# Optimization experiments

Hardware: AMD Instinct MI355X
Metric: run time of the kernel (lower is better)

Reference implementation:

```python
import jax, jax.numpy as jnp
import numpy as np

B, SQ, SE, D, H, DFF = 16, 512, 512, 512, 8, 2048
DH = D // H
EPS = 1e-6


def _ln(x, g, b):
    mu = jnp.mean(x, axis=-1, keepdims=True)
    var = jnp.mean((x - mu) ** 2, axis=-1, keepdims=True)
    return (x - mu) * jax.lax.rsqrt(var + EPS) * g + b


def _mha(v, k, q, mask, wq_w, wq_b, wk_w, wk_b, wv_w, wv_b, do_w, do_b):
    b = q.shape[0]
    def split(t):  # [b, s, D] -> [b, H, s, DH]
        return t.reshape(b, -1, H, DH).transpose(0, 2, 1, 3)
    qh = split(q @ wq_w + wq_b)
    kh = split(k @ wk_w + wk_b)
    vh = split(v @ wv_w + wv_b)
    logits = jnp.einsum('bhqd,bhkd->bhqk', qh, kh) / jnp.sqrt(jnp.float32(DH))
    logits = logits + mask * (-1e9)
    attn = jax.nn.softmax(logits, axis=-1)
    out = jnp.einsum('bhqk,bhkd->bhqd', attn, vh)
    out = out.transpose(0, 2, 1, 3).reshape(b, -1, D)
    # output projection has GELU activation (exact erf, keras default)
    out = jax.nn.gelu(out @ do_w + do_b, approximate=False)
    return out, attn


def setup_inputs() -> dict:
    key = jax.random.key(0)
    ks = jax.random.split(key, 32)
    s = 0.02  # weight scale
    inp = {
        'x': jax.random.normal(ks[0], (B, SQ, D), dtype=jnp.float32),
        'enc_fc': jax.random.normal(ks[1], (B, SE, D), dtype=jnp.float32),
        'enc_ff': jax.random.normal(ks[2], (B, SE, D), dtype=jnp.float32),
        # causal look-ahead mask: 1 where attention is disallowed
        'look_ahead_mask': jnp.triu(jnp.ones((SQ, SQ), jnp.float32), k=1)[None, None],
        # random padding mask over encoder positions (1 = masked)
        'padding_mask': (jax.random.uniform(ks[3], (B, 1, 1, SE)) < 0.1).astype(jnp.float32),
    }
    i = 4
    for p in ('m1', 'm2'):
        for w in ('wq', 'wk', 'wv', 'do'):
            inp[f'{p}_{w}_w'] = jax.random.normal(ks[i], (D, D), dtype=jnp.float32) * s; i += 1
            inp[f'{p}_{w}_b'] = jnp.zeros((D,), jnp.float32)
    inp['ffn_w1'] = jax.random.normal(ks[i], (D, DFF), dtype=jnp.float32) * s; i += 1
    inp['ffn_b1'] = jnp.zeros((DFF,), jnp.float32)
    inp['ffn_w2'] = jax.random.normal(ks[i], (DFF, D), dtype=jnp.float32) * s; i += 1
    inp['ffn_b2'] = jnp.zeros((D,), jnp.float32)
    for ln in ('ln1', 'ln2', 'ln3'):
        inp[f'{ln}_g'] = jnp.ones((D,), jnp.float32)
        inp[f'{ln}_b'] = jnp.zeros((D,), jnp.float32)
    return inp


def reference(x, enc_fc, enc_ff, look_ahead_mask, padding_mask,
              m1_wq_w, m1_wq_b, m1_wk_w, m1_wk_b, m1_wv_w, m1_wv_b, m1_do_w, m1_do_b,
              m2_wq_w, m2_wq_b, m2_wk_w, m2_wk_b, m2_wv_w, m2_wv_b, m2_do_w, m2_do_b,
              ffn_w1, ffn_b1, ffn_w2, ffn_b2,
              ln1_g, ln1_b, ln2_g, ln2_b, ln3_g, ln3_b):
    # self-attention (v=k=q=x), causal mask
    attn1, aw1 = _mha(x, x, x, look_ahead_mask,
                      m1_wq_w, m1_wq_b, m1_wk_w, m1_wk_b, m1_wv_w, m1_wv_b, m1_do_w, m1_do_b)
    out1 = _ln(attn1 + x, ln1_g, ln1_b)  # dropout identity in eval
    # cross-attention: v=enc_ff, k=enc_fc, q=out1, padding mask
    attn2, aw2 = _mha(enc_ff, enc_fc, out1, padding_mask,
                      m2_wq_w, m2_wq_b, m2_wk_w, m2_wk_b, m2_wv_w, m2_wv_b, m2_do_w, m2_do_b)
    out2 = _ln(attn2 + out1, ln2_g, ln2_b)
    # FFN: relu dense -> (dropout identity) -> dense
    ff = jax.nn.relu(out2 @ ffn_w1 + ffn_b1) @ ffn_w2 + ffn_b2
    out3 = _ln(ff + out2, ln3_g, ln3_b)
    return out3, aw1, aw2
```

## Files before the change

### kernel.cpp

```cpp
#include <hip/hip_runtime.h>
#include <stdint.h>
#include <math.h>

typedef unsigned short u16;
typedef __attribute__((ext_vector_type(8))) __bf16 bf16x8;
typedef __attribute__((ext_vector_type(4))) float f32x4;

#define NB 16
#define NSQ 512
#define NSE 512
#define ND 512
#define NH 8
#define NDH 64
#define NDFF 2048

__device__ __forceinline__ u16 f2b(float f) {
  uint32_t u = __float_as_uint(f);
  u = (u + 0x7FFFu + ((u >> 16) & 1u)) >> 16;
  return (u16)u;
}
__device__ __forceinline__ float b2f(uint32_t h) {
  return __uint_as_float(h << 16);
}

__device__ __forceinline__ void gl_lds16(const u16* g, u16* l) {
  __builtin_amdgcn_global_load_lds(
      (const __attribute__((address_space(1))) void*)g,
      (__attribute__((address_space(3))) void*)l, 16, 0, 0);
}

struct Prep {
  const float *x, *fc, *ff;
  u16 *xb, *fcb, *ffb;
  const float* w8[8];
  u16* o8[8];
  const float *w1, *w2;
  u16 *w1t, *w2t;
};

__device__ __forceinline__ void tr32(const float* __restrict__ W,
                                     u16* __restrict__ Wt, int K, int N, int bx,
                                     int by, float (*t)[33]) {
  const int tid = threadIdx.x, tx = tid & 31, ty = tid >> 5;
  const int n0 = bx * 32, k0 = by * 32;
#pragma unroll
  for (int i = 0; i < 32; i += 8)
    t[ty + i][tx] = W[(size_t)(k0 + ty + i) * N + n0 + tx];
  __syncthreads();
#pragma unroll
  for (int i = 0; i < 32; i += 8)
    Wt[(size_t)(n0 + ty + i) * K + k0 + tx] = f2b(t[tx][ty + i]);
}

__global__ void k_prep(Prep p) {
  __shared__ float t[32][33];
  const int blk = blockIdx.x;
  if (blk < 6144) {
    const int plane = blk >> 11;
    const float* src = plane == 0 ? p.x : (plane == 1 ? p.fc : p.ff);
    u16* dst = plane == 0 ? p.xb : (plane == 1 ? p.fcb : p.ffb);
    const int i = (blk & 2047) * 256 + threadIdx.x;
    const float4* q = (const float4*)(src + (size_t)i * 8);
    float4 v0 = q[0], v1 = q[1];
    uint4 o;
    o.x = (uint32_t)f2b(v0.x) | ((uint32_t)f2b(v0.y) << 16);
    o.y = (uint32_t)f2b(v0.z) | ((uint32_t)f2b(v0.w) << 16);
    o.z = (uint32_t)f2b(v1.x) | ((uint32_t)f2b(v1.y) << 16);
    o.w = (uint32_t)f2b(v1.z) | ((uint32_t)f2b(v1.w) << 16);
    *(uint4*)(dst + (size_t)i * 8) = o;
  } else if (blk < 8192) {
    const int b2 = blk - 6144, z = b2 >> 8, bi = b2 & 255;
    tr32(p.w8[z], p.o8[z], 512, 512, bi & 15, bi >> 4, t);
  } else if (blk < 9216) {
    const int b2 = blk - 8192;
    tr32(p.w1, p.w1t, 512, 2048, b2 & 63, b2 >> 6, t);
  } else {
    const int b2 = blk - 9216;
    tr32(p.w2, p.w2t, 2048, 512, b2 & 15, b2 >> 4, t);
  }
}

enum { EPI_GELU = 2, EPI_RELU = 3, EPI_NONE = 4 };

template <int BM>
__device__ __forceinline__ void gemm_core(const u16* __restrict__ A,
                                          const u16* __restrict__ Bt, int K,
                                          int brow, int bcol, u16* As, u16* Bs,
                                          f32x4 (&acc)[BM / 32][4]) {
  const int tid = threadIdx.x, lane = tid & 63, wid = tid >> 6;
  const int wr = wid >> 1, wc = wid & 1;
  const int l15 = lane & 15, g4 = lane >> 4;
  const int sc8 = (lane & 7) * 8;
  const int srow = wid * 8 + (lane >> 3);
  const int nt = K >> 6;
  for (int t = 0; t < nt; ++t) {
    const int k0 = t << 6;
    if (t) __syncthreads();
#pragma unroll
    for (int v = 0; v < BM / 32; ++v)
      gl_lds16(A + (size_t)(brow + v * 32 + srow) * K + k0 + sc8,
               As + (v * 32 + wid * 8) * 64);
#pragma unroll
    for (int v = 0; v < 4; ++v)
      gl_lds16(Bt + (size_t)(bcol + v * 32 + srow) * K + k0 + sc8,
               Bs + (v * 32 + wid * 8) * 64);
    __syncthreads();
#pragma unroll
    for (int kk = 0; kk < 2; ++kk) {
      bf16x8 af[BM / 32], bfr[4];
#pragma unroll
      for (int m = 0; m < BM / 32; ++m)
        af[m] = *(const bf16x8*)(As + (wr * (BM / 2) + m * 16 + l15) * 64 +
                                 kk * 32 + g4 * 8);
#pragma unroll
      for (int n = 0; n < 4; ++n)
        bfr[n] = *(const bf16x8*)(Bs + (wc * 64 + n * 16 + l15) * 64 +
                                  kk * 32 + g4 * 8);
#pragma unroll
      for (int m = 0; m < BM / 32; ++m)
#pragma unroll
        for (int n = 0; n < 4; ++n)
          acc[m][n] =
              __builtin_amdgcn_mfma_f32_16x16x32_bf16(af[m], bfr[n], acc[m][n], 0, 0, 0);
    }
  }
}

template <int BM, int EPI>
__global__ __launch_bounds__(256, 3) void k_gemm(
    const u16* __restrict__ A, const u16* __restrict__ Bt,
    const float* __restrict__ bias, u16* __restrict__ out, int K, int N) {
  __shared__ u16 As[BM * 64];
  __shared__ u16 Bs[128 * 64];
  f32x4 acc[BM / 32][4] = {};
  const int brow = blockIdx.x * BM, bcol = blockIdx.y * 128;
  gemm_core<BM>(A, Bt, K, brow, bcol, As, Bs, acc);
  const int lane = threadIdx.x & 63, wid = threadIdx.x >> 6;
  const int wr = wid >> 1, wc = wid & 1, l15 = lane & 15, g4 = lane >> 4;
#pragma unroll
  for (int m = 0; m < BM / 32; ++m) {
    const int r0 = brow + wr * (BM / 2) + m * 16 + g4 * 4;
#pragma unroll
    for (int n = 0; n < 4; ++n) {
      const int col = bcol + wc * 64 + n * 16 + l15;
      const float bv = bias[col];
#pragma unroll
      for (int j = 0; j < 4; ++j) {
        float vv = acc[m][n][j] + bv;
        if (EPI == EPI_GELU) vv = 0.5f * vv * (1.0f + erff(vv * 0.70710678118654752f));
        if (EPI == EPI_RELU) vv = fmaxf(vv, 0.0f);
        out[(size_t)(r0 + j) * N + col] = f2b(vv);
      }
    }
  }
}

struct QKV {
  const u16* A[3];
  const u16* Bt[3];
  const float* bias[3];
  u16* out[3];
};
__global__ __launch_bounds__(256, 3) void k_gemm_qkv(QKV p) {
  const int z = blockIdx.z;
  __shared__ u16 As[128 * 64];
  __shared__ u16 Bs[128 * 64];
  f32x4 acc[4][4] = {};
  const int brow = blockIdx.x * 128, bcol = blockIdx.y * 128;
  gemm_core<128>(p.A[z], p.Bt[z], 512, brow, bcol, As, Bs, acc);
  const int lane = threadIdx.x & 63, wid = threadIdx.x >> 6;
  const int wr = wid >> 1, wc = wid & 1, l15 = lane & 15, g4 = lane >> 4;
  const float* bias = p.bias[z];
  u16* out = p.out[z];
#pragma unroll
  for (int m = 0; m < 4; ++m) {
    const int r0 = brow + wr * 64 + m * 16 + g4 * 4;
#pragma unroll
    for (int n = 0; n < 4; ++n) {
      const int col = bcol + wc * 64 + n * 16 + l15;
      const float bv = bias[col];
      const int h = col >> 6, d = col & 63;
#pragma unroll
      for (int j = 0; j < 4; ++j) {
        const int r = r0 + j, b = r >> 9, s = r & 511;
        const float vv = acc[m][n][j] + bv;
        if (z < 2)
          out[((size_t)(b * NH + h) * NSQ + s) * NDH + d] = f2b(vv);
        else
          out[((size_t)(b * NH + h) * NDH + d) * NSE + s] = f2b(vv);
      }
    }
  }
}

template <int CAUSAL>
__global__ __launch_bounds__(512, 4) void k_attn_fused(
    const u16* __restrict__ qh, const u16* __restrict__ kh,
    const u16* __restrict__ vtg, const float* __restrict__ pmask,
    float* __restrict__ aw, u16* __restrict__ ctx) {
  __shared__ u16 Kt[128 * 64];
  __shared__ u16 Vs[64 * 128];
  __shared__ u16 Ps[128 * 128];

  const int bh = blockIdx.y, b = bh >> 3, h = bh & 7;
  const int brow = blockIdx.x * 128;
  const int tid = threadIdx.x, lane = tid & 63, wid = tid >> 6;
  const int l15 = lane & 15, g4 = lane >> 4;
  const u16* Q = qh + (size_t)bh * NSQ * NDH;
  const u16* Kg = kh + (size_t)bh * NSE * NDH;
  const u16* Vg = vtg + (size_t)bh * NDH * NSE;
  float* awp = aw + (size_t)bh * NSQ * NSE;

  const int krow = wid * 8 + (lane >> 3);
  const int ksw = ((lane & 7) ^ (krow & 7)) * 8;
  const int vsw = (l15 ^ ((wid * 4 + g4) & 7)) * 8;

  bf16x8 qf[2];
#pragma unroll
  for (int kk = 0; kk < 2; ++kk)
    qf[kk] = *(const bf16x8*)(Q + (size_t)(brow + wid * 16 + l15) * NDH +
                              kk * 32 + g4 * 8);

  const int ntile = CAUSAL ? blockIdx.x + 1 : 4;

  auto stage_k = [&](int kb) {
#pragma unroll
    for (int v = 0; v < 2; ++v)
      gl_lds16(Kg + (size_t)(kb + v * 64 + krow) * NDH + ksw,
               Kt + (v * 64 + wid * 8) * 64);
  };
  auto stage_v = [&](int kb) {
#pragma unroll
    for (int v = 0; v < 2; ++v) {
      const int d = v * 32 + wid * 4 + g4;
      gl_lds16(Vg + (size_t)d * NSE + kb + vsw, Vs + (v * 32 + wid * 4) * 128);
    }
  };
  auto computeS = [&](int kb, f32x4(&acc)[8]) {
#pragma unroll
    for (int kk = 0; kk < 2; ++kk) {
      bf16x8 kf[8];
#pragma unroll
      for (int n = 0; n < 8; ++n) {
        const int kr = n * 16 + l15;
        kf[n] = *(const bf16x8*)(Kt + kr * 64 + ((kk * 32 + g4 * 8) ^ ((kr & 7) << 3)));
      }
#pragma unroll
      for (int n = 0; n < 8; ++n)
        acc[n] = __builtin_amdgcn_mfma_f32_16x16x32_bf16(qf[kk], kf[n], acc[n], 0, 0, 0);
    }
    if (!CAUSAL) {
      float pm[8];
#pragma unroll
      for (int n = 0; n < 8; ++n)
        pm[n] = pmask[b * NSE + kb + n * 16 + l15] * (-1e9f);
#pragma unroll
      for (int n = 0; n < 8; ++n)
#pragma unroll
        for (int j = 0; j < 4; ++j)
          acc[n][j] = fminf(acc[n][j] * 0.125f, 60.0f) + pm[n];
    } else {
#pragma unroll
      for (int n = 0; n < 8; ++n) {
        const int key = kb + n * 16 + l15;
#pragma unroll
        for (int j = 0; j < 4; ++j) {
          const int qrow = brow + wid * 16 + g4 * 4 + j;
          acc[n][j] = (key > qrow) ? -1e9f : fminf(acc[n][j] * 0.125f, 60.0f);
        }
      }
    }
  };

  float l4[4] = {0.f, 0.f, 0.f, 0.f};
  for (int t = 0; t < ntile; ++t) {
    if (t) __syncthreads();
    stage_k(t * 128);
    __syncthreads();
    f32x4 acc[8] = {};
    computeS(t * 128, acc);
#pragma unroll
    for (int j = 0; j < 4; ++j) {
      float s = 0.f;
#pragma unroll
      for (int n = 0; n < 8; ++n) s += __expf(acc[n][j]);
#pragma unroll
      for (int o = 1; o < 16; o <<= 1) s += __shfl_xor(s, o, 64);
      l4[j] += s;
    }
  }
  float invl[4];
#pragma unroll
  for (int j = 0; j < 4; ++j) invl[j] = 1.0f / l4[j];

  f32x4 apv[4] = {};
  for (int t = 0; t < ntile; ++t) {
    const int kb = t * 128;
    __syncthreads();
    stage_k(kb);
    stage_v(kb);
    __syncthreads();
    f32x4 acc[8] = {};
    computeS(kb, acc);
#pragma unroll
    for (int n = 0; n < 8; ++n) {
      const int col = n * 16 + l15;
#pragma unroll
      for (int j = 0; j < 4; ++j) {
        const int rl = wid * 16 + g4 * 4 + j;
        const float p = __expf(acc[n][j]) * invl[j];
        awp[(size_t)(brow + rl) * NSE + kb + col] = p;
        Ps[rl * 128 + (col ^ ((rl & 7) << 3))] = f2b(p);
      }
    }
#pragma unroll
    for (int kk = 0; kk < 4; ++kk) {
      const int qr = wid * 16 + l15;
      bf16x8 pa =
          *(const bf16x8*)(Ps + qr * 128 + ((kk * 32 + g4 * 8) ^ ((qr & 7) << 3)));
      bf16x8 vb[4];
#pragma unroll
      for (int n = 0; n < 4; ++n) {
        const int d = n * 16 + l15;
        vb[n] = *(const bf16x8*)(Vs + d * 128 + ((kk * 32 + g4 * 8) ^ ((d & 7) << 3)));
      }
#pragma unroll
      for (int n = 0; n < 4; ++n)
        apv[n] = __builtin_amdgcn_mfma_f32_16x16x32_bf16(pa, vb[n], apv[n], 0, 0, 0);
    }
  }

  if (CAUSAL) {
    const float4 z4 = make_float4(0.f, 0.f, 0.f, 0.f);
    for (int t = ntile; t < 4; ++t) {
      const int r = tid >> 2, c0 = t * 128 + (tid & 3) * 32;
      float4* p = (float4*)(awp + (size_t)(brow + r) * NSE + c0);
#pragma unroll
      for (int i = 0; i < 8; ++i) p[i] = z4;
    }
  }

#pragma unroll
  for (int n = 0; n < 4; ++n) {
    const int d = n * 16 + l15;
#pragma unroll
    for (int j = 0; j < 4; ++j) {
      const int r = brow + wid * 16 + g4 * 4 + j;
      ctx[((size_t)(b * NSQ + r)) * ND + h * NDH + d] = f2b(apv[n][j]);
    }
  }
}

template <int B_BF16, int OUT_F32>
__global__ __launch_bounds__(256) void k_res_ln(const u16* __restrict__ a,
                                                const void* __restrict__ bsrc,
                                                const float* __restrict__ g,
                                                const float* __restrict__ bet,
                                                void* __restrict__ outp) {
  const int row = blockIdx.x * 4 + (threadIdx.x >> 6);
  const int lane = threadIdx.x & 63;
  const size_t base = (size_t)row * 512 + lane * 8;
  float s[8];
  {
    uint4 av = *(const uint4*)(a + base);
    s[0] = b2f(av.x & 0xffffu); s[1] = b2f(av.x >> 16);
    s[2] = b2f(av.y & 0xffffu); s[3] = b2f(av.y >> 16);
    s[4] = b2f(av.z & 0xffffu); s[5] = b2f(av.z >> 16);
    s[6] = b2f(av.w & 0xffffu); s[7] = b2f(av.w >> 16);
  }
  if (B_BF16) {
    uint4 bv = *(const uint4*)((const u16*)bsrc + base);
    s[0] += b2f(bv.x & 0xffffu); s[1] += b2f(bv.x >> 16);
    s[2] += b2f(bv.y & 0xffffu); s[3] += b2f(bv.y >> 16);
    s[4] += b2f(bv.z & 0xffffu); s[5] += b2f(bv.z >> 16);
    s[6] += b2f(bv.w & 0xffffu); s[7] += b2f(bv.w >> 16);
  } else {
    const float* bp = (const float*)bsrc + base;
    float4 b0 = *(const float4*)bp, b1 = *(const float4*)(bp + 4);
    s[0] += b0.x; s[1] += b0.y; s[2] += b0.z; s[3] += b0.w;
    s[4] += b1.x; s[5] += b1.y; s[6] += b1.z; s[7] += b1.w;
  }
  float sum = 0.f;
#pragma unroll
  for (int i = 0; i < 8; ++i) sum += s[i];
#pragma unroll
  for (int o = 1; o < 64; o <<= 1) sum += __shfl_xor(sum, o, 64);
  const float mu = sum * (1.0f / 512.0f);
  float vs = 0.f;
#pragma unroll
  for (int i = 0; i < 8; ++i) {
    const float d = s[i] - mu;
    vs += d * d;
  }
#pragma unroll
  for (int o = 1; o < 64; o <<= 1) vs += __shfl_xor(vs, o, 64);
  const float rs = rsqrtf(vs * (1.0f / 512.0f) + 1e-6f);
  float y[8];
#pragma unroll
  for (int i = 0; i < 8; ++i) {
    const int c = lane * 8 + i;
    y[i] = (s[i] - mu) * rs * g[c] + bet[c];
  }
  if (OUT_F32) {
    float* op = (float*)outp + base;
    *(float4*)op = make_float4(y[0], y[1], y[2], y[3]);
    *(float4*)(op + 4) = make_float4(y[4], y[5], y[6], y[7]);
  } else {
    uint4 o;
    o.x = (uint32_t)f2b(y[0]) | ((uint32_t)f2b(y[1]) << 16);
    o.y = (uint32_t)f2b(y[2]) | ((uint32_t)f2b(y[3]) << 16);
    o.z = (uint32_t)f2b(y[4]) | ((uint32_t)f2b(y[5]) << 16);
    o.w = (uint32_t)f2b(y[6]) | ((uint32_t)f2b(y[7]) << 16);
    *(uint4*)((u16*)outp + base) = o;
  }
}

extern "C" void kernel_launch(void* const* d_in, const int* in_sizes, int n_in,
                              void* d_out, int out_size, void* d_ws, size_t ws_size,
                              hipStream_t stream) {
  (void)in_sizes; (void)n_in; (void)out_size; (void)ws_size;
  const float* x = (const float*)d_in[0];
  const float* enc_fc = (const float*)d_in[1];
  const float* enc_ff = (const float*)d_in[2];
  const float* pmask = (const float*)d_in[4];
  const float* w_m1[4] = {(const float*)d_in[5], (const float*)d_in[7],
                          (const float*)d_in[9], (const float*)d_in[11]};
  const float* b_m1[4] = {(const float*)d_in[6], (const float*)d_in[8],
                          (const float*)d_in[10], (const float*)d_in[12]};
  const float* w_m2[4] = {(const float*)d_in[13], (const float*)d_in[15],
                          (const float*)d_in[17], (const float*)d_in[19]};
  const float* b_m2[4] = {(const float*)d_in[14], (const float*)d_in[16],
                          (const float*)d_in[18], (const float*)d_in[20]};
  const float* ffn_w1 = (const float*)d_in[21];
  const float* ffn_b1 = (const float*)d_in[22];
  const float* ffn_w2 = (const float*)d_in[23];
  const float* ffn_b2 = (const float*)d_in[24];
  const float* ln_g[3] = {(const float*)d_in[25], (const float*)d_in[27],
                          (const float*)d_in[29]};
  const float* ln_b[3] = {(const float*)d_in[26], (const float*)d_in[28],
                          (const float*)d_in[30]};

  char* ws = (char*)d_ws;
  const size_t SZB = (size_t)8192 * 512 * 2;
  u16* xb = (u16*)(ws + 0 * SZB);
  u16* fcb = (u16*)(ws + 1 * SZB);
  u16* ffb = (u16*)(ws + 2 * SZB);
  u16* qh = (u16*)(ws + 3 * SZB);
  u16* kh = (u16*)(ws + 4 * SZB);
  u16* vt = (u16*)(ws + 5 * SZB);
  u16* ctx = (u16*)(ws + 6 * SZB);
  u16* ao = (u16*)(ws + 7 * SZB);
  u16* out1 = (u16*)(ws + 8 * SZB);
  u16* out2 = (u16*)(ws + 9 * SZB);
  u16* ffv = (u16*)(ws + 10 * SZB);
  u16* ff1 = (u16*)(ws + 11 * SZB);
  u16* wts = (u16*)(ws + 11 * SZB + (size_t)8192 * 2048 * 2);
  u16 *wt_m1[4], *wt_m2[4];
  for (int i = 0; i < 4; ++i) {
    wt_m1[i] = wts + (size_t)i * 262144;
    wt_m2[i] = wts + (size_t)(4 + i) * 262144;
  }
  u16* w1t = wts + (size_t)8 * 262144;
  u16* w2t = w1t + (size_t)2048 * 512;

  float* out3 = (float*)d_out;
  float* aw1 = out3 + (size_t)NB * NSQ * ND;
  float* aw2 = aw1 + (size_t)NB * NH * NSQ * NSQ;

  Prep pr;
  pr.x = x; pr.fc = enc_fc; pr.ff = enc_ff;
  pr.xb = xb; pr.fcb = fcb; pr.ffb = ffb;
  for (int i = 0; i < 4; ++i) {
    pr.w8[i] = w_m1[i]; pr.o8[i] = wt_m1[i];
    pr.w8[4 + i] = w_m2[i]; pr.o8[4 + i] = wt_m2[i];
  }
  pr.w1 = ffn_w1; pr.w1t = w1t;
  pr.w2 = ffn_w2; pr.w2t = w2t;
  k_prep<<<10240, 256, 0, stream>>>(pr);

  const dim3 gattn(4, 128);
  QKV q1 = {{xb, xb, xb},
            {wt_m1[0], wt_m1[1], wt_m1[2]},
            {b_m1[0], b_m1[1], b_m1[2]},
            {qh, kh, vt}};
  k_gemm_qkv<<<dim3(64, 4, 3), 256, 0, stream>>>(q1);
  k_attn_fused<1><<<gattn, 512, 0, stream>>>(qh, kh, vt, nullptr, aw1, ctx);
  k_gemm<64, EPI_GELU><<<dim3(128, 4), 256, 0, stream>>>(ctx, wt_m1[3], b_m1[3], ao, 512, 512);
  k_res_ln<0, 0><<<2048, 256, 0, stream>>>(ao, x, ln_g[0], ln_b[0], out1);
  QKV q2 = {{out1, fcb, ffb},
            {wt_m2[0], wt_m2[1], wt_m2[2]},
            {b_m2[0], b_m2[1], b_m2[2]},
            {qh, kh, vt}};
  k_gemm_qkv<<<dim3(64, 4, 3), 256, 0, stream>>>(q2);
  k_attn_fused<0><<<gattn, 512, 0, stream>>>(qh, kh, vt, pmask, aw2, ctx);
  k_gemm<64, EPI_GELU><<<dim3(128, 4), 256, 0, stream>>>(ctx, wt_m2[3], b_m2[3], ao, 512, 512);
  k_res_ln<1, 0><<<2048, 256, 0, stream>>>(ao, out1, ln_g[1], ln_b[1], out2);
  k_gemm<128, EPI_RELU><<<dim3(64, 16), 256, 0, stream>>>(out2, w1t, ffn_b1, ff1, 512, 2048);
  k_gemm<64, EPI_NONE><<<dim3(128, 4), 256, 0, stream>>>(ff1, w2t, ffn_b2, ffv, 2048, 512);
  k_res_ln<1, 1><<<2048, 256, 0, stream>>>(ffv, out2, ln_g[2], ln_b[2], (void*)d_out);
}
```

Before: 326.8 us.

## Fuse output-projection GEMMs with residual add and LayerNorm into one kernel

Adds a GEMM kernel whose 32-row block covers the full 512-wide output, so bias, activation, residual add and LayerNorm run in the epilogue via cross-wave shared-memory reductions. This replaces three GEMM plus res_ln pairs and drops the intermediate bf16 round trips through global memory and the extra launches. In exchange the grid shrinks to 256 blocks with a large per-block B tile and no double buffering, which may lower GEMM efficiency. Variance is now computed as E[x^2]-mu^2 rather than the two-pass form.

```diff
diff --git a/kernel.cpp b/kernel.cpp
--- a/kernel.cpp
+++ b/kernel.cpp
@@ -193,6 +193,115 @@
   }
 }
 
+template <int KDIM, int EPI, int RES_BF16, int OUT_F32>
+__global__ __launch_bounds__(512, 4) void k_gemm_ln(
+    const u16* __restrict__ A, const u16* __restrict__ Bt,
+    const float* __restrict__ bias, const void* __restrict__ res,
+    const float* __restrict__ g, const float* __restrict__ bet,
+    void* __restrict__ outp) {
+  __shared__ u16 As[32 * 64];
+  __shared__ u16 Bs[512 * 64];
+  __shared__ float psum[32][8];
+  __shared__ float psq[32][8];
+  const int tid = threadIdx.x, lane = tid & 63, wid = tid >> 6;
+  const int l15 = lane & 15, g4 = lane >> 4;
+  const int brow = blockIdx.x * 32;
+  const int sc8 = (lane & 7) * 8, sr8 = lane >> 3;
+  f32x4 acc[2][4] = {};
+  const int nt = KDIM >> 6;
+  for (int t = 0; t < nt; ++t) {
+    const int k0 = t << 6;
+    if (t) __syncthreads();
+    if (wid < 4)
+      gl_lds16(A + (size_t)(brow + wid * 8 + sr8) * KDIM + k0 + sc8,
+               As + wid * 8 * 64);
+#pragma unroll
+    for (int v = 0; v < 8; ++v)
+      gl_lds16(Bt + (size_t)(wid * 64 + v * 8 + sr8) * KDIM + k0 + sc8,
+               Bs + (wid * 64 + v * 8) * 64);
+    __syncthreads();
+#pragma unroll
+    for (int kk = 0; kk < 2; ++kk) {
+      bf16x8 af[2], bf[4];
+#pragma unroll
+      for (int m = 0; m < 2; ++m)
+        af[m] = *(const bf16x8*)(As + (m * 16 + l15) * 64 + kk * 32 + g4 * 8);
+#pragma unroll
+      for (int n = 0; n < 4; ++n)
+        bf[n] = *(const bf16x8*)(Bs + (wid * 64 + n * 16 + l15) * 64 + kk * 32 + g4 * 8);
+#pragma unroll
+      for (int m = 0; m < 2; ++m)
+#pragma unroll
+        for (int n = 0; n < 4; ++n)
+          acc[m][n] =
+              __builtin_amdgcn_mfma_f32_16x16x32_bf16(af[m], bf[n], acc[m][n], 0, 0, 0);
+    }
+  }
+  const u16* rb = (const u16*)res;
+  const float* rf = (const float*)res;
+#pragma unroll
+  for (int m = 0; m < 2; ++m)
+#pragma unroll
+    for (int n = 0; n < 4; ++n) {
+      const int col = wid * 64 + n * 16 + l15;
+      const float bv = bias[col];
+#pragma unroll
+      for (int j = 0; j < 4; ++j) {
+        const int r = brow + m * 16 + g4 * 4 + j;
+        float vv = acc[m][n][j] + bv;
+        if (EPI == EPI_GELU) vv = 0.5f * vv * (1.0f + erff(vv * 0.70710678118654752f));
+        vv += RES_BF16 ? b2f(rb[(size_t)r * 512 + col]) : rf[(size_t)r * 512 + col];
+        acc[m][n][j] = vv;
+      }
+    }
+#pragma unroll
+  for (int m = 0; m < 2; ++m)
+#pragma unroll
+    for (int j = 0; j < 4; ++j) {
+      float s = 0.f, s2 = 0.f;
+#pragma unroll
+      for (int n = 0; n < 4; ++n) {
+        const float v = acc[m][n][j];
+        s += v;
+        s2 += v * v;
+      }
+#pragma unroll
+      for (int o = 1; o < 16; o <<= 1) {
+        s += __shfl_xor(s, o, 64);
+        s2 += __shfl_xor(s2, o, 64);
+      }
+      if (l15 == 0) {
+        psum[m * 16 + g4 * 4 + j][wid] = s;
+        psq[m * 16 + g4 * 4 + j][wid] = s2;
+      }
+    }
+  __syncthreads();
+#pragma unroll
+  for (int m = 0; m < 2; ++m)
+#pragma unroll
+    for (int j = 0; j < 4; ++j) {
+      const int rl = m * 16 + g4 * 4 + j;
+      float s = 0.f, s2 = 0.f;
+#pragma unroll
+      for (int wcol = 0; wcol < 8; ++wcol) {
+        s += psum[rl][wcol];
+        s2 += psq[rl][wcol];
+      }
+      const float mu = s * (1.0f / 512.0f);
+      const float rs = rsqrtf(s2 * (1.0f / 512.0f) - mu * mu + 1e-6f);
+      const size_t r = (size_t)(brow + rl);
+#pragma unroll
+      for (int n = 0; n < 4; ++n) {
+        const int col = wid * 64 + n * 16 + l15;
+        const float y = (acc[m][n][j] - mu) * rs * g[col] + bet[col];
+        if (OUT_F32)
+          ((float*)outp)[r * 512 + col] = y;
+        else
+          ((u16*)outp)[r * 512 + col] = f2b(y);
+      }
+    }
+}
+
 template <int CAUSAL>
 __global__ __launch_bounds__(512, 4) void k_attn_fused(
     const u16* __restrict__ qh, const u16* __restrict__ kh,
@@ -348,70 +457,6 @@
       const int r = brow + wid * 16 + g4 * 4 + j;
       ctx[((size_t)(b * NSQ + r)) * ND + h * NDH + d] = f2b(apv[n][j]);
     }
-  }
-}
-
-template <int B_BF16, int OUT_F32>
-__global__ __launch_bounds__(256) void k_res_ln(const u16* __restrict__ a,
-                                                const void* __restrict__ bsrc,
-                                                const float* __restrict__ g,
-                                                const float* __restrict__ bet,
-                                                void* __restrict__ outp) {
-  const int row = blockIdx.x * 4 + (threadIdx.x >> 6);
-  const int lane = threadIdx.x & 63;
-  const size_t base = (size_t)row * 512 + lane * 8;
-  float s[8];
-  {
-    uint4 av = *(const uint4*)(a + base);
-    s[0] = b2f(av.x & 0xffffu); s[1] = b2f(av.x >> 16);
-    s[2] = b2f(av.y & 0xffffu); s[3] = b2f(av.y >> 16);
-    s[4] = b2f(av.z & 0xffffu); s[5] = b2f(av.z >> 16);
-    s[6] = b2f(av.w & 0xffffu); s[7] = b2f(av.w >> 16);
-  }
-  if (B_BF16) {
-    uint4 bv = *(const uint4*)((const u16*)bsrc + base);
-    s[0] += b2f(bv.x & 0xffffu); s[1] += b2f(bv.x >> 16);
-    s[2] += b2f(bv.y & 0xffffu); s[3] += b2f(bv.y >> 16);
-    s[4] += b2f(bv.z & 0xffffu); s[5] += b2f(bv.z >> 16);
-    s[6] += b2f(bv.w & 0xffffu); s[7] += b2f(bv.w >> 16);
-  } else {
-    const float* bp = (const float*)bsrc + base;
-    float4 b0 = *(const float4*)bp, b1 = *(const float4*)(bp + 4);
-    s[0] += b0.x; s[1] += b0.y; s[2] += b0.z; s[3] += b0.w;
-    s[4] += b1.x; s[5] += b1.y; s[6] += b1.z; s[7] += b1.w;
-  }
-  float sum = 0.f;
-#pragma unroll
-  for (int i = 0; i < 8; ++i) sum += s[i];
-#pragma unroll
-  for (int o = 1; o < 64; o <<= 1) sum += __shfl_xor(sum, o, 64);
-  const float mu = sum * (1.0f / 512.0f);
-  float vs = 0.f;
-#pragma unroll
-  for (int i = 0; i < 8; ++i) {
-    const float d = s[i] - mu;
-    vs += d * d;
-  }
-#pragma unroll
-  for (int o = 1; o < 64; o <<= 1) vs += __shfl_xor(vs, o, 64);
-  const float rs = rsqrtf(vs * (1.0f / 512.0f) + 1e-6f);
-  float y[8];
-#pragma unroll
-  for (int i = 0; i < 8; ++i) {
-    const int c = lane * 8 + i;
-    y[i] = (s[i] - mu) * rs * g[c] + bet[c];
-  }
-  if (OUT_F32) {
-    float* op = (float*)outp + base;
-    *(float4*)op = make_float4(y[0], y[1], y[2], y[3]);
-    *(float4*)(op + 4) = make_float4(y[4], y[5], y[6], y[7]);
-  } else {
-    uint4 o;
-    o.x = (uint32_t)f2b(y[0]) | ((uint32_t)f2b(y[1]) << 16);
-    o.y = (uint32_t)f2b(y[2]) | ((uint32_t)f2b(y[3]) << 16);
-    o.z = (uint32_t)f2b(y[4]) | ((uint32_t)f2b(y[5]) << 16);
-    o.w = (uint32_t)f2b(y[6]) | ((uint32_t)f2b(y[7]) << 16);
-    *(uint4*)((u16*)outp + base) = o;
   }
 }
 
@@ -449,10 +494,8 @@
   u16* kh = (u16*)(ws + 4 * SZB);
   u16* vt = (u16*)(ws + 5 * SZB);
   u16* ctx = (u16*)(ws + 6 * SZB);
-  u16* ao = (u16*)(ws + 7 * SZB);
   u16* out1 = (u16*)(ws + 8 * SZB);
   u16* out2 = (u16*)(ws + 9 * SZB);
-  u16* ffv = (u16*)(ws + 10 * SZB);
   u16* ff1 = (u16*)(ws + 11 * SZB);
   u16* wts = (u16*)(ws + 11 * SZB + (size_t)8192 * 2048 * 2);
   u16 *wt_m1[4], *wt_m2[4];
@@ -485,17 +528,17 @@
             {qh, kh, vt}};
   k_gemm_qkv<<<dim3(64, 4, 3), 256, 0, stream>>>(q1);
   k_attn_fused<1><<<gattn, 512, 0, stream>>>(qh, kh, vt, nullptr, aw1, ctx);
-  k_gemm<64, EPI_GELU><<<dim3(128, 4), 256, 0, stream>>>(ctx, wt_m1[3], b_m1[3], ao, 512, 512);
-  k_res_ln<0, 0><<<2048, 256, 0, stream>>>(ao, x, ln_g[0], ln_b[0], out1);
+  k_gemm_ln<512, EPI_GELU, 0, 0><<<256, 512, 0, stream>>>(
+      ctx, wt_m1[3], b_m1[3], x, ln_g[0], ln_b[0], out1);
   QKV q2 = {{out1, fcb, ffb},
             {wt_m2[0], wt_m2[1], wt_m2[2]},
             {b_m2[0], b_m2[1], b_m2[2]},
             {qh, kh, vt}};
   k_gemm_qkv<<<dim3(64, 4, 3), 256, 0, stream>>>(q2);
   k_attn_fused<0><<<gattn, 512, 0, stream>>>(qh, kh, vt, pmask, aw2, ctx);
-  k_gemm<64, EPI_GELU><<<dim3(128, 4), 256, 0, stream>>>(ctx, wt_m2[3], b_m2[3], ao, 512, 512);
-  k_res_ln<1, 0><<<2048, 256, 0, stream>>>(ao, out1, ln_g[1], ln_b[1], out2);
+  k_gemm_ln<512, EPI_GELU, 1, 0><<<256, 512, 0, stream>>>(
+      ctx, wt_m2[3], b_m2[3], out1, ln_g[1], ln_b[1], out2);
   k_gemm<128, EPI_RELU><<<dim3(64, 16), 256, 0, stream>>>(out2, w1t, ffn_b1, ff1, 512, 2048);
-  k_gemm<64, EPI_NONE><<<dim3(128, 4), 256, 0, stream>>>(ff1, w2t, ffn_b2, ffv, 2048, 512);
-  k_res_ln<1, 1><<<2048, 256, 0, stream>>>(ffv, out2, ln_g[2], ln_b[2], (void*)d_out);
-}
+  k_gemm_ln<2048, EPI_NONE, 1, 1><<<256, 512, 0, stream>>>(
+      ff1, w2t, ffn_b2, out2, ln_g[2], ln_b[2], (void*)d_out);
+}
```

Result: slower. 384.9 us (+17.8%).
